# Kernel tuning notes

Hardware: AMD Instinct MI355X
Metric: run time of the kernel (lower is better)

The kernel has to match this reference:

```python
import jax, jax.numpy as jnp
import numpy as np

N = 16384
E = 262144
IN = 512
H = 64
K = 8


def setup_inputs() -> dict:
    key = jax.random.key(0)
    ks = jax.random.split(key, 16)
    def lin(k, fan_in, fan_out):
        # xavier_uniform
        lim = float(np.sqrt(6.0 / (fan_in + fan_out)))
        return jax.random.uniform(k, (fan_in, fan_out), jnp.float32, -lim, lim)
    inp = {
        'x': jax.random.normal(ks[0], (N, IN), jnp.float32),
        'edge_index': jax.random.randint(ks[1], (2, E), 0, N, jnp.int64) if jax.config.read('jax_enable_x64') else jax.random.randint(ks[1], (2, E), 0, N, jnp.int32),
        'W1': lin(ks[2], IN, H), 'b1': jnp.zeros((H,), jnp.float32),
        'W2': lin(ks[3], H, H), 'b2': jnp.zeros((H,), jnp.float32),
        'W3': lin(ks[4], H, H), 'b3': jnp.zeros((H,), jnp.float32),
        'W4': lin(ks[5], H, H), 'b4': jnp.zeros((H,), jnp.float32),
        'Wg1': lin(ks[6], H, H), 'bg1': jnp.zeros((H,), jnp.float32),
        'Wg2': lin(ks[7], H, H), 'bg2': jnp.zeros((H,), jnp.float32),
    }
    return inp


def reference(x, edge_index, W1, b1, W2, b2, W3, b3, W4, b4, Wg1, bg1, Wg2, bg2):
    n = x.shape[0]
    row, col = edge_index[0], edge_index[1]
    # symmetric-normalized Laplacian action: L v = v - D^-1/2 A D^-1/2 v
    deg = jax.ops.segment_sum(jnp.ones(row.shape[0], x.dtype), row, num_segments=n)
    dinv = jnp.where(deg > 0, jax.lax.rsqrt(jnp.maximum(deg, 1e-30)), 0.0)
    # spectral embedding MLP stack (dropout=0 -> identity)
    h = jnp.maximum(x @ W1 + b1, 0.0) @ W2 + b2
    h = jnp.maximum(h @ W3 + b3, 0.0) @ W4 + b4
    g = jnp.maximum(h @ Wg1 + bg1, 0.0) @ Wg2 + bg2  # [N, H]
    msg = (dinv[row] * dinv[col])[:, None] * g[col]   # [E, H]
    agg = jax.ops.segment_sum(msg, row, num_segments=n)
    filtered = g - agg                                 # L @ gft_x
    sim = filtered @ filtered.T                        # [N, N], dominant cost
    topk_vals, topk_idx = jax.lax.top_k(sim, K)        # [N, K]
    src = jnp.repeat(jnp.arange(n, dtype=topk_idx.dtype), K)
    new_edge_index = jnp.stack([src, topk_idx.reshape(-1)])  # [2, N*K]
    return topk_vals, new_edge_index
```

## Files before the change

### kernel.cpp

```cpp
#include <hip/hip_runtime.h>
#include <hip/hip_bf16.h>

#define N_NODES 16384
#define E_EDGES 262144
#define IN_DIM 512
#define KKEEP 56

#define AGG_SCALE 1099511627776.0
#define AGG_INV   (1.0/1099511627776.0)

typedef __attribute__((ext_vector_type(8))) short bf16x8;
typedef __attribute__((ext_vector_type(4))) float f32x4;

__device__ __forceinline__ int detect64(const void* __restrict__ ei) {
    const unsigned long long v = ((const unsigned long long*)ei)[threadIdx.x & 63];
    return __all(v < 16384ull) ? 1 : 0;
}

__device__ __forceinline__ int edge_at(const void* __restrict__ ei, int is64, int pos) {
    return is64 ? (int)(((const long long*)ei)[pos]) : ((const int*)ei)[pos];
}

__global__ __launch_bounds__(256) void deg_kernel(const void* __restrict__ ei,
                                                  int* __restrict__ deg) {
    const int is64 = detect64(ei);
    int e = blockIdx.x * 256 + threadIdx.x;
    int r = edge_at(ei, is64, e);
    if (r >= 0 && r < N_NODES) atomicAdd(&deg[r], 1);
}

__global__ __launch_bounds__(256) void scan_kernel(const int* __restrict__ deg, int* __restrict__ offs,
                                                   float* __restrict__ dinv) {
    __shared__ int part[257];
    const int t = threadIdx.x;
    const int base = t * 64;
    int s = 0;
    #pragma unroll 4
    for (int i = 0; i < 64; ++i) s += deg[base + i];
    part[t + 1] = s;
    if (t == 0) part[0] = 0;
    __syncthreads();
    if (t == 0) {
        int acc = 0;
        for (int i = 1; i <= 256; ++i) { acc += part[i]; part[i] = acc; }
    }
    __syncthreads();
    int run = part[t];
    for (int i = 0; i < 64; ++i) {
        const int d = deg[base + i];
        offs[base + i] = run; run += d;
        dinv[base + i] = (d > 0) ? __fdiv_rn(1.0f, __fsqrt_rn((float)d)) : 0.0f;
    }
    if (t == 255) offs[N_NODES] = run;
}

__global__ __launch_bounds__(256) void scatter_kernel(
    const void* __restrict__ ei,
    const int* __restrict__ offs, int* __restrict__ cursor, int* __restrict__ ecol_s)
{
    const int is64 = detect64(ei);
    int e = blockIdx.x * 256 + threadIdx.x;
    int r  = edge_at(ei, is64, e);
    if (r < 0 || r >= N_NODES) return;
    int cc = edge_at(ei, is64, E_EDGES + e);
    int pos = atomicAdd(&cursor[r], 1);
    ecol_s[offs[r] + pos] = (cc >= 0 && cc < N_NODES) ? cc : -1;
}

__device__ __forceinline__ void dense_layer32(float (*hsw)[64], int c,
                                              const float* __restrict__ WP,
                                              const float* __restrict__ BP,
                                              bool relu, bool last,
                                              float* __restrict__ gout, int n0)
{
    float s0 = 0.0f, s1 = 0.0f, s2 = 0.0f, s3 = 0.0f;
    #pragma unroll 4
    for (int k = 0; k < 64; k += 4) {
        const float4 h0 = *(const float4*)&hsw[0][k];
        const float4 h1 = *(const float4*)&hsw[1][k];
        const float4 h2 = *(const float4*)&hsw[2][k];
        const float4 h3 = *(const float4*)&hsw[3][k];
        const float w0 = WP[k * 64 + c];
        const float w1 = WP[(k + 1) * 64 + c];
        const float w2 = WP[(k + 2) * 64 + c];
        const float w3 = WP[(k + 3) * 64 + c];
        s0 = fmaf(h0.x, w0, s0); s0 = fmaf(h0.y, w1, s0); s0 = fmaf(h0.z, w2, s0); s0 = fmaf(h0.w, w3, s0);
        s1 = fmaf(h1.x, w0, s1); s1 = fmaf(h1.y, w1, s1); s1 = fmaf(h1.z, w2, s1); s1 = fmaf(h1.w, w3, s1);
        s2 = fmaf(h2.x, w0, s2); s2 = fmaf(h2.y, w1, s2); s2 = fmaf(h2.z, w2, s2); s2 = fmaf(h2.w, w3, s2);
        s3 = fmaf(h3.x, w0, s3); s3 = fmaf(h3.y, w1, s3); s3 = fmaf(h3.z, w2, s3); s3 = fmaf(h3.w, w3, s3);
    }
    const float bv = BP[c];
    s0 += bv; s1 += bv; s2 += bv; s3 += bv;
    if (relu) { s0 = fmaxf(s0, 0.0f); s1 = fmaxf(s1, 0.0f); s2 = fmaxf(s2, 0.0f); s3 = fmaxf(s3, 0.0f); }
    __syncthreads();
    if (last) {
        gout[(size_t)(n0 + 0) * 64 + c] = s0;
        gout[(size_t)(n0 + 1) * 64 + c] = s1;
        gout[(size_t)(n0 + 2) * 64 + c] = s2;
        gout[(size_t)(n0 + 3) * 64 + c] = s3;
    } else {
        hsw[0][c] = s0; hsw[1][c] = s1; hsw[2][c] = s2; hsw[3][c] = s3;
    }
    __syncthreads();
}

__global__ __launch_bounds__(256) void mlp_kernel(
    const float* __restrict__ x,
    const float* __restrict__ W1, const float* __restrict__ b1,
    const float* __restrict__ W2, const float* __restrict__ b2,
    const float* __restrict__ W3, const float* __restrict__ b3,
    const float* __restrict__ W4, const float* __restrict__ b4,
    const float* __restrict__ Wg1, const float* __restrict__ bg1,
    const float* __restrict__ Wg2, const float* __restrict__ bg2,
    float* __restrict__ g32)
{
    __shared__ float hs[4][4][64];
    const int w = threadIdx.x >> 6;
    const int c = threadIdx.x & 63;
    const int n0 = blockIdx.x * 16 + w * 4;

    float a0 = 0.0f, a1 = 0.0f, a2 = 0.0f, a3 = 0.0f;
    const float* xp = x + (size_t)n0 * IN_DIM;
    #pragma unroll 2
    for (int k = 0; k < IN_DIM; k += 4) {
        const float4 x0 = *(const float4*)(xp + k);
        const float4 x1 = *(const float4*)(xp + IN_DIM + k);
        const float4 x2 = *(const float4*)(xp + 2 * IN_DIM + k);
        const float4 x3 = *(const float4*)(xp + 3 * IN_DIM + k);
        const float w0 = W1[k * 64 + c];
        const float w1 = W1[(k + 1) * 64 + c];
        const float w2 = W1[(k + 2) * 64 + c];
        const float w3 = W1[(k + 3) * 64 + c];
        a0 = fmaf(x0.x, w0, a0); a0 = fmaf(x0.y, w1, a0); a0 = fmaf(x0.z, w2, a0); a0 = fmaf(x0.w, w3, a0);
        a1 = fmaf(x1.x, w0, a1); a1 = fmaf(x1.y, w1, a1); a1 = fmaf(x1.z, w2, a1); a1 = fmaf(x1.w, w3, a1);
        a2 = fmaf(x2.x, w0, a2); a2 = fmaf(x2.y, w1, a2); a2 = fmaf(x2.z, w2, a2); a2 = fmaf(x2.w, w3, a2);
        a3 = fmaf(x3.x, w0, a3); a3 = fmaf(x3.y, w1, a3); a3 = fmaf(x3.z, w2, a3); a3 = fmaf(x3.w, w3, a3);
    }
    const float bv = b1[c];
    hs[w][0][c] = fmaxf(a0 + bv, 0.0f);
    hs[w][1][c] = fmaxf(a1 + bv, 0.0f);
    hs[w][2][c] = fmaxf(a2 + bv, 0.0f);
    hs[w][3][c] = fmaxf(a3 + bv, 0.0f);
    __syncthreads();

    dense_layer32(hs[w], c, W2, b2, false, false, g32, n0);
    dense_layer32(hs[w], c, W3, b3, true,  false, g32, n0);
    dense_layer32(hs[w], c, W4, b4, false, false, g32, n0);
    dense_layer32(hs[w], c, Wg1, bg1, true, false, g32, n0);
    dense_layer32(hs[w], c, Wg2, bg2, false, true, g32, n0);
}

__global__ __launch_bounds__(256) void aggcsr_kernel(
    const int* __restrict__ offs, const int* __restrict__ ecol_s,
    const float* __restrict__ dinv, const float* __restrict__ g32,
    float* __restrict__ F32, short* __restrict__ Fb)
{
    const int r = (blockIdx.x << 2) + (threadIdx.x >> 6);
    const int h = threadIdx.x & 63;
    const float dr = dinv[r];
    const int b = offs[r], e2 = offs[r + 1];
    long long sum = 0;
    #pragma unroll 8
    for (int i = b; i < e2; ++i) {
        const int cc = ecol_s[i];
        if (cc < 0) continue;
        const float m = __fmul_rn(__fmul_rn(dr, dinv[cc]), g32[((size_t)cc << 6) + h]);
        sum += __double2ll_rn((double)m * AGG_SCALE);
    }
    const float a = (float)((double)sum * AGG_INV);
    const int idx = (r << 6) + h;
    const float f = g32[idx] - a;
    F32[idx] = f;
    __hip_bfloat16 hb = __float2bfloat16(f);
    Fb[idx] = *(short*)&hb;
}

__device__ __forceinline__ void ins6(unsigned* k, unsigned x) {
    const unsigned r0 = max(k[0], x);
    k[5] = min(k[4], max(k[5], x));
    k[4] = min(k[3], max(k[4], x));
    k[3] = min(k[2], max(k[3], x));
    k[2] = min(k[1], max(k[2], x));
    k[1] = min(k[0], max(k[1], x));
    k[0] = r0;
}

__global__ __launch_bounds__(256) void screen_kernel(
    const short* __restrict__ Fb, unsigned* __restrict__ cand)
{
    __shared__ short Bt[2][128 * 64];
    const int l = threadIdx.x & 63;
    const int w = threadIdx.x >> 6;
    const int rb = blockIdx.x >> 1;
    const int sp = blockIdx.x & 1;
    const int r0 = rb * 64 + w * 16;
    const int c0 = sp * 8192;

    const short* ap = Fb + ((size_t)(r0 + (l & 15)) << 6) + ((l >> 4) << 3);
    const bf16x8 a0 = *(const bf16x8*)(ap);
    const bf16x8 a1 = *(const bf16x8*)(ap + 32);

    unsigned keys[4][6];
    #pragma unroll
    for (int r = 0; r < 4; ++r)
        #pragma unroll
        for (int t = 0; t < 6; ++t) keys[r][t] = 0u;

    const int scol = threadIdx.x & 127;
    const int jb = (threadIdx.x >> 7) * 4;
    const short* gsrc0 = Fb + ((size_t)(c0 + scol) << 6) + jb * 8;

    bf16x8 st[4];
    #pragma unroll
    for (int j = 0; j < 4; ++j) st[j] = *(const bf16x8*)(gsrc0 + j * 8);
    #pragma unroll
    for (int j = 0; j < 4; ++j)
        *(bf16x8*)(&Bt[0][scol * 64 + (((jb + j) ^ (scol & 7)) << 3)]) = st[j];
    #pragma unroll
    for (int j = 0; j < 4; ++j) st[j] = *(const bf16x8*)(gsrc0 + (1 << 13) + j * 8);
    __syncthreads();

    const unsigned invb = 0x80000000u | (unsigned)(16383 - c0 - (l & 15));
    const int g0 = (l >> 4) ^ (l & 7);
    const int g1 = ((l >> 4) + 4) ^ (l & 7);
    int cur = 0;

    #pragma unroll 1
    for (int t = 0; t < 64; ++t) {
        const short* B = &Bt[cur][0];
        bf16x8 bf[16];
        #pragma unroll
        for (int s = 0; s < 8; ++s) {
            const int C = s * 16 + (l & 15);
            bf[2 * s]     = *(const bf16x8*)(B + C * 64 + (g0 << 3));
            bf[2 * s + 1] = *(const bf16x8*)(B + C * 64 + (g1 << 3));
        }
        if (t + 1 < 64) {
            #pragma unroll
            for (int j = 0; j < 4; ++j)
                *(bf16x8*)(&Bt[cur ^ 1][scol * 64 + (((jb + j) ^ (scol & 7)) << 3)]) = st[j];
        }
        if (t + 2 < 64) {
            const short* gs = gsrc0 + ((size_t)(t + 2) << 13);
            #pragma unroll
            for (int j = 0; j < 4; ++j) st[j] = *(const bf16x8*)(gs + j * 8);
        }
        #pragma unroll
        for (int s = 0; s < 8; ++s) {
            f32x4 acc = {0.0f, 0.0f, 0.0f, 0.0f};
            acc = __builtin_amdgcn_mfma_f32_16x16x32_bf16(a0, bf[2 * s], acc, 0, 0, 0);
            acc = __builtin_amdgcn_mfma_f32_16x16x32_bf16(a1, bf[2 * s + 1], acc, 0, 0, 0);
            const unsigned xv = invb - (unsigned)((t << 7) + (s << 4));
            #pragma unroll
            for (int r = 0; r < 4; ++r) {
                const unsigned key = (__float_as_uint(acc[r]) & 0xFFFFC000u) ^ xv;
                ins6(keys[r], key);
            }
        }
        __syncthreads();
        cur ^= 1;
    }

    #pragma unroll
    for (int r = 0; r < 4; ++r) {
        const int row = r0 + ((l >> 4) << 2) + r;
        unsigned* cp = cand + ((size_t)(sp * N_NODES + row)) * 96 + (l & 15) * 6;
        #pragma unroll
        for (int t = 0; t < 6; ++t) cp[t] = keys[r][t];
    }
}

__global__ __launch_bounds__(512) void refine2_kernel(
    const float* __restrict__ F, const unsigned* __restrict__ cand,
    float* __restrict__ out)
{
    __shared__ unsigned skey[192];
    __shared__ int clist[64];
    __shared__ float scand[KKEEP * 68];
    const int t = threadIdx.x;

    #pragma unroll 1
    for (int row = blockIdx.x; row < N_NODES; row += 2048) {
        if (t < 192) {
            const int sp = (t >= 96) ? 1 : 0;
            const int slot = t - 96 * sp;
            skey[t] = cand[((size_t)(sp * N_NODES + row)) * 96 + slot];
        }
        __syncthreads();

        if (t < 64) {
            const unsigned k0 = skey[t], k1 = skey[t + 64], k2 = skey[t + 128];
            unsigned long long lo = 0, hi = 0xFFFFFFFFull;
            while (hi - lo > 1) {
                const unsigned mid = (unsigned)((lo + hi) >> 1);
                const int cnt = __popcll(__ballot(k0 >= mid)) +
                                __popcll(__ballot(k1 >= mid)) +
                                __popcll(__ballot(k2 >= mid));
                if (cnt >= KKEEP) lo = mid; else hi = mid;
            }
            const unsigned thr = (unsigned)lo;
            const unsigned long long m0 = __ballot(k0 >= thr);
            const unsigned long long m1 = __ballot(k1 >= thr);
            const unsigned long long m2 = __ballot(k2 >= thr);
            const unsigned long long ltm = (1ull << t) - 1ull;
            const int b1 = __popcll(m0), b2 = b1 + __popcll(m1);
            if (k0 >= thr) clist[__popcll(m0 & ltm)]      = 16383 - (int)(k0 & 0x3FFFu);
            if (k1 >= thr) clist[b1 + __popcll(m1 & ltm)] = 16383 - (int)(k1 & 0x3FFFu);
            if (k2 >= thr) clist[b2 + __popcll(m2 & ltm)] = 16383 - (int)(k2 & 0x3FFFu);
        }
        __syncthreads();

        if (t < KKEEP * 8) {
            const int g = t >> 3, sub = t & 7;
            const float* src = F + ((size_t)clist[g] << 6) + sub * 8;
            *(float4*)(&scand[g * 68 + sub * 8])     = *(const float4*)(src);
            *(float4*)(&scand[g * 68 + sub * 8 + 4]) = *(const float4*)(src + 4);
        }
        __syncthreads();

        float val = -3.4e38f; int idx = 1 << 30;
        if (t < KKEEP) {
            idx = clist[t];
            const float* fp = &scand[t * 68];
            const float* frp = F + ((size_t)row << 6);
            float acc = 0.0f;
            #pragma unroll 4
            for (int j = 0; j < 16; ++j) {
                const float4 a = *(const float4*)(frp + 4 * j);
                const float4 b = *(const float4*)(fp + 4 * j);
                acc = fmaf(a.x, b.x, acc);
                acc = fmaf(a.y, b.y, acc);
                acc = fmaf(a.z, b.z, acc);
                acc = fmaf(a.w, b.w, acc);
            }
            val = acc;
        }
        if (t < 64) {
            #pragma unroll 1
            for (int it = 0; it < 8; ++it) {
                float bv = val; int bi = idx;
                #pragma unroll
                for (int off = 32; off > 0; off >>= 1) {
                    const float ov = __shfl_xor(bv, off);
                    const int   oi = __shfl_xor(bi, off);
                    if (ov > bv || (ov == bv && oi < bi)) { bv = ov; bi = oi; }
                }
                if (t == 0) {
                    out[(size_t)row * 8 + it]          = bv;
                    out[131072 + (size_t)row * 8 + it] = (float)row;
                    out[262144 + (size_t)row * 8 + it] = (float)bi;
                }
                if (idx == bi) val = -3.4e38f;
            }
        }
        __syncthreads();
    }
}

__global__ void canary_kernel(float* out, float code) {
    out[0] = code;
}

extern "C" void kernel_launch(void* const* d_in, const int* in_sizes, int n_in,
                              void* d_out, int out_size, void* d_ws, size_t ws_size,
                              hipStream_t stream)
{
    const float* x   = (const float*)d_in[0];
    const void*  ei  = d_in[1];
    const float* W1  = (const float*)d_in[2];  const float* b1  = (const float*)d_in[3];
    const float* W2  = (const float*)d_in[4];  const float* b2  = (const float*)d_in[5];
    const float* W3  = (const float*)d_in[6];  const float* b3  = (const float*)d_in[7];
    const float* W4  = (const float*)d_in[8];  const float* b4  = (const float*)d_in[9];
    const float* Wg1 = (const float*)d_in[10]; const float* bg1 = (const float*)d_in[11];
    const float* Wg2 = (const float*)d_in[12]; const float* bg2 = (const float*)d_in[13];
    float* out = (float*)d_out;

    char* ws = (char*)d_ws;
    float* g32 = (float*)(ws);
    float* F32 = (float*)(ws + ((size_t)4 << 20));
    short* Fb  = (short*)(ws + ((size_t)8 << 20));
    unsigned* cand = (unsigned*)(ws + ((size_t)10 << 20));
    int*   ecol_s = (int*)(ws + ((size_t)10 << 20));
    int*   offs   = (int*)(ws + ((size_t)11 << 20));
    int*   deg    = (int*)(ws + ((size_t)23 << 20));
    int*   cursor = (int*)(ws + ((size_t)23 << 20) + (1u << 16));
    float* dinvf  = (float*)(ws + ((size_t)23 << 20) + (2u << 16));

    const size_t NEEDED = ((size_t)23 << 20) + (3u << 16);
    if (ws_size < NEEDED || n_in < 14) {
        canary_kernel<<<1, 1, 0, stream>>>(out, ws_size < NEEDED ? 5000.0f : 3000.0f);
        return;
    }

    hipMemsetAsync(deg, 0, 2 * N_NODES * sizeof(int), stream);

    deg_kernel<<<E_EDGES / 256, 256, 0, stream>>>(ei, deg);
    scan_kernel<<<1, 256, 0, stream>>>(deg, offs, dinvf);
    scatter_kernel<<<E_EDGES / 256, 256, 0, stream>>>(ei, offs, cursor, ecol_s);
    mlp_kernel<<<N_NODES / 16, 256, 0, stream>>>(x, W1, b1, W2, b2, W3, b3, W4, b4, Wg1, bg1, Wg2, bg2, g32);
    aggcsr_kernel<<<N_NODES / 4, 256, 0, stream>>>(offs, ecol_s, dinvf, g32, F32, Fb);
    screen_kernel<<<512, 256, 0, stream>>>(Fb, cand);
    refine2_kernel<<<2048, 512, 0, stream>>>(F32, cand, out);
}
```

Before: 447.4 us.

## Process two rows per block in refine kernel with register-prefetched candidate keys

Splits each 512-thread refine block into two 256-thread halves that each handle a separate row, halving the grid. Candidate keys for the next row are prefetched into registers while the current row is processed. The trailing barrier is dropped and candidate gathers use wider per-thread loads. The aim is to hide global load latency and cut idle threads; the cost is more shared memory per block and reliance on barrier ordering for correctness.

```diff
diff --git a/kernel.cpp b/kernel.cpp
--- a/kernel.cpp
+++ b/kernel.cpp
@@ -274,22 +274,33 @@
     const float* __restrict__ F, const unsigned* __restrict__ cand,
     float* __restrict__ out)
 {
-    __shared__ unsigned skey[192];
-    __shared__ int clist[64];
-    __shared__ float scand[KKEEP * 68];
-    const int t = threadIdx.x;
+    __shared__ unsigned skey[2][192];
+    __shared__ int clist[2][64];
+    __shared__ float scand[2][KKEEP * 68];
+    const int tid = threadIdx.x;
+    const int half = tid >> 8;
+    const int th = tid & 255;
+
+    const int ksp = (th >= 96) ? 1 : 0;
+    const int kslot = th - 96 * ksp;
+
+    unsigned kreg = 0u;
+    {
+        const int row0 = blockIdx.x * 2 + half;
+        if (th < 192) kreg = cand[((size_t)(ksp * N_NODES + row0)) * 96 + kslot];
+    }
 
     #pragma unroll 1
-    for (int row = blockIdx.x; row < N_NODES; row += 2048) {
-        if (t < 192) {
-            const int sp = (t >= 96) ? 1 : 0;
-            const int slot = t - 96 * sp;
-            skey[t] = cand[((size_t)(sp * N_NODES + row)) * 96 + slot];
-        }
+    for (int i = 0; i < 8; ++i) {
+        const int row = blockIdx.x * 2 + half + i * 2048;
+        if (th < 192) skey[half][th] = kreg;
         __syncthreads();
 
-        if (t < 64) {
-            const unsigned k0 = skey[t], k1 = skey[t + 64], k2 = skey[t + 128];
+        if (i + 1 < 8 && th < 192)
+            kreg = cand[((size_t)(ksp * N_NODES + (row + 2048))) * 96 + kslot];
+
+        if (th < 64) {
+            const unsigned k0 = skey[half][th], k1 = skey[half][th + 64], k2 = skey[half][th + 128];
             unsigned long long lo = 0, hi = 0xFFFFFFFFull;
             while (hi - lo > 1) {
                 const unsigned mid = (unsigned)((lo + hi) >> 1);
@@ -302,26 +313,28 @@
             const unsigned long long m0 = __ballot(k0 >= thr);
             const unsigned long long m1 = __ballot(k1 >= thr);
             const unsigned long long m2 = __ballot(k2 >= thr);
-            const unsigned long long ltm = (1ull << t) - 1ull;
+            const unsigned long long ltm = (1ull << th) - 1ull;
             const int b1 = __popcll(m0), b2 = b1 + __popcll(m1);
-            if (k0 >= thr) clist[__popcll(m0 & ltm)]      = 16383 - (int)(k0 & 0x3FFFu);
-            if (k1 >= thr) clist[b1 + __popcll(m1 & ltm)] = 16383 - (int)(k1 & 0x3FFFu);
-            if (k2 >= thr) clist[b2 + __popcll(m2 & ltm)] = 16383 - (int)(k2 & 0x3FFFu);
+            if (k0 >= thr) clist[half][__popcll(m0 & ltm)]      = 16383 - (int)(k0 & 0x3FFFu);
+            if (k1 >= thr) clist[half][b1 + __popcll(m1 & ltm)] = 16383 - (int)(k1 & 0x3FFFu);
+            if (k2 >= thr) clist[half][b2 + __popcll(m2 & ltm)] = 16383 - (int)(k2 & 0x3FFFu);
         }
         __syncthreads();
 
-        if (t < KKEEP * 8) {
-            const int g = t >> 3, sub = t & 7;
-            const float* src = F + ((size_t)clist[g] << 6) + sub * 8;
-            *(float4*)(&scand[g * 68 + sub * 8])     = *(const float4*)(src);
-            *(float4*)(&scand[g * 68 + sub * 8 + 4]) = *(const float4*)(src + 4);
+        if (th < KKEEP * 4) {
+            const int g = th >> 2, sub = th & 3;
+            const float* src = F + ((size_t)clist[half][g] << 6) + sub * 16;
+            float* dst = &scand[half][g * 68 + sub * 16];
+            #pragma unroll
+            for (int j = 0; j < 4; ++j)
+                *(float4*)(dst + 4 * j) = *(const float4*)(src + 4 * j);
         }
         __syncthreads();
 
         float val = -3.4e38f; int idx = 1 << 30;
-        if (t < KKEEP) {
-            idx = clist[t];
-            const float* fp = &scand[t * 68];
+        if (th < KKEEP) {
+            idx = clist[half][th];
+            const float* fp = &scand[half][th * 68];
             const float* frp = F + ((size_t)row << 6);
             float acc = 0.0f;
             #pragma unroll 4
@@ -335,7 +348,7 @@
             }
             val = acc;
         }
-        if (t < 64) {
+        if (th < 64) {
             #pragma unroll 1
             for (int it = 0; it < 8; ++it) {
                 float bv = val; int bi = idx;
@@ -345,7 +358,7 @@
                     const int   oi = __shfl_xor(bi, off);
                     if (ov > bv || (ov == bv && oi < bi)) { bv = ov; bi = oi; }
                 }
-                if (t == 0) {
+                if (th == 0) {
                     out[(size_t)row * 8 + it]          = bv;
                     out[131072 + (size_t)row * 8 + it] = (float)row;
                     out[262144 + (size_t)row * 8 + it] = (float)bi;
@@ -353,7 +366,6 @@
                 if (idx == bi) val = -3.4e38f;
             }
         }
-        __syncthreads();
     }
 }
 
@@ -400,5 +412,5 @@
     mlp_kernel<<<N_NODES / 16, 256, 0, stream>>>(x, W1, b1, W2, b2, W3, b3, W4, b4, Wg1, bg1, Wg2, bg2, g32);
     aggcsr_kernel<<<N_NODES / 4, 256, 0, stream>>>(offs, ecol_s, dinvf, g32, F32, Fb);
     screen_kernel<<<512, 256, 0, stream>>>(Fb, cand);
-    refine2_kernel<<<2048, 512, 0, stream>>>(F32, cand, out);
-}
+    refine2_kernel<<<1024, 512, 0, stream>>>(F32, cand, out);
+}
```

Measured after the change: 391.4 us. -12.5%, faster.
